# Performance work log

Hardware: AMD Instinct MI355X
Metric: run time of the kernel (lower is better)

Reference implementation:

```python
import jax, jax.numpy as jnp
import numpy as np

H = 2048          # hidden_size
E = 16            # n_routed_experts
K = 4             # num_experts_per_tok
I = 1408          # moe_intermediate_size
SH_I = 2 * I      # shared experts intermediate (n_shared_experts * moe_intermediate_size)
B, S = 1, 1024


def setup_inputs() -> dict:
    key = jax.random.key(0)
    ks = jax.random.split(key, 9)
    sc_h = 1.0 / np.sqrt(H)
    sc_i = 1.0 / np.sqrt(I)
    return {
        "hidden_states": jax.random.normal(ks[0], (B, S, H), dtype=jnp.float32),
        "w_gate": jax.random.normal(ks[1], (E, H), dtype=jnp.float32) * sc_h,
        "wg": jax.random.normal(ks[2], (E, H, I), dtype=jnp.float32) * sc_h,  # gate_proj per expert
        "wu": jax.random.normal(ks[3], (E, H, I), dtype=jnp.float32) * sc_h,  # up_proj per expert
        "wd": jax.random.normal(ks[4], (E, I, H), dtype=jnp.float32) * sc_i,  # down_proj per expert
        "sg": jax.random.normal(ks[5], (H, SH_I), dtype=jnp.float32) * sc_h,  # shared gate_proj
        "su": jax.random.normal(ks[6], (H, SH_I), dtype=jnp.float32) * sc_h,  # shared up_proj
        "sd": jax.random.normal(ks[7], (SH_I, H), dtype=jnp.float32) * (1.0 / np.sqrt(SH_I)),
    }


def reference(hidden_states, w_gate, wg, wu, wd, sg, su, sd):
    b, s, h = hidden_states.shape
    x = hidden_states.reshape(-1, h)                      # [T, H]
    T = x.shape[0]

    # --- router: softmax (fp32) -> topk -> scatter-add weights into [T, E] ---
    logits = x @ w_gate.T                                 # [T, E]
    probs = jax.nn.softmax(logits.astype(jnp.float32), axis=-1)
    top_w, top_i = jax.lax.top_k(probs, K)                # [T, K]
    routing_weight = jnp.zeros((T, E), dtype=probs.dtype)
    routing_weight = routing_weight.at[jnp.arange(T)[:, None], top_i].add(top_w)  # scatter_add_

    # --- routed experts (grouped SwiGLU MLPs), weighted combine ---
    g = jnp.einsum('th,ehi->tei', x, wg)                  # [T, E, I]
    u = jnp.einsum('th,ehi->tei', x, wu)
    act = jax.nn.silu(g) * u                              # [T, E, I]
    routed = jnp.einsum('te,tei,eih->th', routing_weight, act, wd)  # [T, H]

    # --- shared experts (always on) ---
    shared = (jax.nn.silu(x @ sg) * (x @ su)) @ sd        # [T, H]

    out = (routed + shared).astype(hidden_states.dtype)
    return out.reshape(b, s, h)
```

## Files before the change

kernel.cpp:

```cpp
#include <hip/hip_runtime.h>
#include <hip/hip_bf16.h>
#include <stdint.h>

#define T_NUM 1024
#define H_DIM 2048
#define E_NUM 16
#define TOPK 4
#define I_DIM 1408
#define SHI_DIM 2816

typedef __attribute__((ext_vector_type(4))) float f32x4;
typedef __attribute__((ext_vector_type(8))) short bf16x8;
typedef __attribute__((ext_vector_type(4))) short s16x4;

static __device__ __forceinline__ short f2bf(float f) {
    __hip_bfloat16 h = __float2bfloat16(f);
    return __builtin_bit_cast(short, h);
}

__global__ void router_kernel(const float* __restrict__ x, const float* __restrict__ wgate,
                              int* __restrict__ top_e, float* __restrict__ top_w) {
    const int t = blockIdx.x;
    const int tid = threadIdx.x;
    __shared__ float xsh[H_DIM];
    const float* xr = x + (size_t)t * H_DIM;
    for (int h = tid; h < H_DIM; h += 256) xsh[h] = xr[h];
    __syncthreads();

    const int e = tid >> 4;
    const int j = tid & 15;
    const float* wr = wgate + (size_t)e * H_DIM;
    float acc = 0.f;
    for (int h = j; h < H_DIM; h += 16) acc += xsh[h] * wr[h];
    #pragma unroll
    for (int m = 8; m >= 1; m >>= 1) acc += __shfl_down(acc, m, 16);

    __shared__ float logits[E_NUM];
    if (j == 0) logits[e] = acc;
    __syncthreads();

    if (tid == 0) {
        float mx = logits[0];
        #pragma unroll
        for (int i = 1; i < E_NUM; ++i) mx = fmaxf(mx, logits[i]);
        float p[E_NUM]; float s = 0.f;
        #pragma unroll
        for (int i = 0; i < E_NUM; ++i) { p[i] = expf(logits[i] - mx); s += p[i]; }
        const float inv = 1.f / s;
        #pragma unroll
        for (int i = 0; i < E_NUM; ++i) p[i] *= inv;
        for (int k = 0; k < TOPK; ++k) {
            float best = -1.f; int bi = 0;
            #pragma unroll
            for (int i = 0; i < E_NUM; ++i) if (p[i] > best) { best = p[i]; bi = i; }
            top_e[t * TOPK + k] = bi;
            top_w[t * TOPK + k] = best;
            p[bi] = -2.f;
        }
    }
}

__global__ void perm_kernel(const int* __restrict__ top_e,
                            int* __restrict__ offs, int* __restrict__ perm) {
    __shared__ int cnt[256][E_NUM];
    __shared__ int base[E_NUM];
    const int tid = threadIdx.x;
    int c[E_NUM];
    #pragma unroll
    for (int i = 0; i < E_NUM; ++i) c[i] = 0;
    for (int s = tid * 16; s < tid * 16 + 16; ++s) c[top_e[s]]++;
    #pragma unroll
    for (int i = 0; i < E_NUM; ++i) cnt[tid][i] = c[i];
    __syncthreads();
    if (tid < E_NUM) {
        int run = 0;
        for (int b = 0; b < 256; ++b) { int v = cnt[b][tid]; cnt[b][tid] = run; run += v; }
        base[tid] = run;
    }
    __syncthreads();
    if (tid == 0) {
        int run = 0;
        for (int e2 = 0; e2 < E_NUM; ++e2) { int v = base[e2]; base[e2] = run; offs[e2] = run; run += v; }
        offs[E_NUM] = run;
    }
    __syncthreads();
    int run[E_NUM];
    #pragma unroll
    for (int i = 0; i < E_NUM; ++i) run[i] = base[i] + cnt[tid][i];
    for (int s = tid * 16; s < tid * 16 + 16; ++s) {
        int e2 = top_e[s];
        perm[run[e2]++] = s;
    }
}

template<int MODE>
__global__ __launch_bounds__(256, 2) void moe_gemm(
    const float* __restrict__ A, int lda, int Kdim,
    const float* __restrict__ B1g, const float* __restrict__ B2g, int ldb,
    float* __restrict__ Out, int ldo,
    const int* __restrict__ perm, const int* __restrict__ offs,
    const float* __restrict__ top_w)
{
    constexpr int NB = (MODE == 0 || MODE == 1) ? 2 : 1;
    constexpr int BM = 128, BN = 128, BK = 32, KP = 40;
    __shared__ short As[2][BM * KP];
    __shared__ short Bs[2][NB * BN * KP];
    __shared__ int   rows_a[BM];
    __shared__ int   rows_o[BM];
    __shared__ float w_m[BM];

    const int tid = threadIdx.x;
    const int nt = blockIdx.x, mt = blockIdx.y, e = blockIdx.z;

    int off = 0, cnt = T_NUM;
    const float* B1 = B1g;
    const float* B2 = B2g;
    if constexpr (MODE == 0) {
        off = offs[e]; cnt = offs[e + 1] - off;
        if (mt * BM >= cnt) return;
        B1 = B1g + (size_t)e * H_DIM * I_DIM;
        B2 = B2g + (size_t)e * H_DIM * I_DIM;
    }
    if constexpr (MODE == 2) {
        off = offs[e]; cnt = offs[e + 1] - off;
        if (mt * BM >= cnt) return;
        B1 = B1g + (size_t)e * I_DIM * H_DIM;
    }

    if (tid < BM) {
        const int gm = mt * BM + tid;
        if constexpr (MODE == 0) {
            int s = perm[off + (gm < cnt ? gm : cnt - 1)];
            rows_a[tid] = s >> 2; rows_o[tid] = s; w_m[tid] = 1.f;
        } else if constexpr (MODE == 2) {
            int s = perm[off + (gm < cnt ? gm : cnt - 1)];
            rows_a[tid] = s; rows_o[tid] = s >> 2; w_m[tid] = top_w[s];
        } else {
            rows_a[tid] = gm; rows_o[tid] = gm; w_m[tid] = 1.f;
        }
    }
    __syncthreads();

    f32x4 aReg[4];
    float bReg[NB][4][4];

    auto gload = [&](int kt) {
        const int k0 = kt * BK;
        #pragma unroll
        for (int it = 0; it < 4; ++it) {
            const int q = it * 256 + tid;
            const int m = q >> 3, kq = (q & 7) * 4;
            aReg[it] = *reinterpret_cast<const f32x4*>(A + (size_t)rows_a[m] * lda + k0 + kq);
        }
        #pragma unroll
        for (int it = 0; it < 4; ++it) {
            const int q = it * 256 + tid;
            const int n = q & 127, kb = (q >> 7) * 4;
            const float* p1 = B1 + (size_t)(k0 + kb) * ldb + (size_t)nt * BN + n;
            #pragma unroll
            for (int dk = 0; dk < 4; ++dk) bReg[0][it][dk] = p1[(size_t)dk * ldb];
            if constexpr (NB == 2) {
                const float* p2 = B2 + (size_t)(k0 + kb) * ldb + (size_t)nt * BN + n;
                #pragma unroll
                for (int dk = 0; dk < 4; ++dk) bReg[1][it][dk] = p2[(size_t)dk * ldb];
            }
        }
    };

    auto swrite = [&](int buf) {
        #pragma unroll
        for (int it = 0; it < 4; ++it) {
            const int q = it * 256 + tid;
            const int m = q >> 3, kq = (q & 7) * 4;
            s16x4 v = { f2bf(aReg[it][0]), f2bf(aReg[it][1]), f2bf(aReg[it][2]), f2bf(aReg[it][3]) };
            *reinterpret_cast<s16x4*>(&As[buf][m * KP + kq]) = v;
        }
        #pragma unroll
        for (int it = 0; it < 4; ++it) {
            const int q = it * 256 + tid;
            const int n = q & 127, kb = (q >> 7) * 4;
            #pragma unroll
            for (int mat = 0; mat < NB; ++mat) {
                s16x4 v = { f2bf(bReg[mat][it][0]), f2bf(bReg[mat][it][1]),
                            f2bf(bReg[mat][it][2]), f2bf(bReg[mat][it][3]) };
                *reinterpret_cast<s16x4*>(&Bs[buf][mat * BN * KP + n * KP + kb]) = v;
            }
        }
    };

    f32x4 acc1[4][4], acc2[4][4];
    #pragma unroll
    for (int i = 0; i < 4; ++i)
        #pragma unroll
        for (int j = 0; j < 4; ++j) { acc1[i][j] = (f32x4)0.f; acc2[i][j] = (f32x4)0.f; }

    const int lane = tid & 63;
    const int wr = (tid >> 6) >> 1, wc = (tid >> 6) & 1;
    const int lrow = lane & 15;
    const int lko = (lane >> 4) * 8;

    auto compute = [&](int buf) {
        bf16x8 af[4];
        #pragma unroll
        for (int mi = 0; mi < 4; ++mi)
            af[mi] = *reinterpret_cast<const bf16x8*>(&As[buf][(wr * 64 + mi * 16 + lrow) * KP + lko]);
        #pragma unroll
        for (int ni = 0; ni < 4; ++ni) {
            const int brow = (wc * 64 + ni * 16 + lrow) * KP + lko;
            bf16x8 b1 = *reinterpret_cast<const bf16x8*>(&Bs[buf][brow]);
            #pragma unroll
            for (int mi = 0; mi < 4; ++mi)
                acc1[mi][ni] = __builtin_amdgcn_mfma_f32_16x16x32_bf16(af[mi], b1, acc1[mi][ni], 0, 0, 0);
            if constexpr (NB == 2) {
                bf16x8 b2 = *reinterpret_cast<const bf16x8*>(&Bs[buf][BN * KP + brow]);
                #pragma unroll
                for (int mi = 0; mi < 4; ++mi)
                    acc2[mi][ni] = __builtin_amdgcn_mfma_f32_16x16x32_bf16(af[mi], b2, acc2[mi][ni], 0, 0, 0);
            }
        }
    };

    const int NK = Kdim / BK;
    gload(0);
    int cur = 0;
    for (int kt = 0; kt < NK; ++kt) {
        swrite(cur);
        __syncthreads();
        if (kt + 1 < NK) gload(kt + 1);
        compute(cur);
        cur ^= 1;
    }

    #pragma unroll
    for (int mi = 0; mi < 4; ++mi) {
        #pragma unroll
        for (int j = 0; j < 4; ++j) {
            const int ml = wr * 64 + mi * 16 + (lane >> 4) * 4 + j;
            const int gm = mt * BM + ml;
            if constexpr (MODE == 0 || MODE == 2) { if (gm >= cnt) continue; }
            const int orow = rows_o[ml];
            const float wsc = w_m[ml];
            #pragma unroll
            for (int ni = 0; ni < 4; ++ni) {
                const int n = nt * BN + wc * 64 + ni * 16 + (lane & 15);
                const float v1 = acc1[mi][ni][j];
                if constexpr (NB == 2) {
                    const float u = acc2[mi][ni][j];
                    const float s = v1 / (1.f + __expf(-v1));
                    Out[(size_t)orow * ldo + n] = s * u;
                } else if constexpr (MODE == 2) {
                    atomicAdd(&Out[(size_t)orow * ldo + n], v1 * wsc);
                } else {
                    Out[(size_t)orow * ldo + n] = v1;
                }
            }
        }
    }
}

extern "C" void kernel_launch(void* const* d_in, const int* in_sizes, int n_in,
                              void* d_out, int out_size, void* d_ws, size_t ws_size,
                              hipStream_t stream) {
    const float* x     = (const float*)d_in[0];
    const float* wgate = (const float*)d_in[1];
    const float* wg    = (const float*)d_in[2];
    const float* wu    = (const float*)d_in[3];
    const float* wd    = (const float*)d_in[4];
    const float* sg    = (const float*)d_in[5];
    const float* su    = (const float*)d_in[6];
    const float* sd    = (const float*)d_in[7];
    float* out = (float*)d_out;

    uintptr_t p = (uintptr_t)d_ws;
    auto alloc = [&](size_t bytes) {
        p = (p + 255) & ~(uintptr_t)255;
        void* r = (void*)p; p += bytes; return r;
    };
    int*   top_e = (int*)alloc((size_t)T_NUM * TOPK * sizeof(int));
    float* top_w = (float*)alloc((size_t)T_NUM * TOPK * sizeof(float));
    int*   offs  = (int*)alloc((E_NUM + 1) * sizeof(int));
    int*   perm  = (int*)alloc((size_t)T_NUM * TOPK * sizeof(int));
    float* act_r = (float*)alloc((size_t)T_NUM * TOPK * I_DIM * sizeof(float));
    float* act_s = (float*)alloc((size_t)T_NUM * SHI_DIM * sizeof(float));

    router_kernel<<<T_NUM, 256, 0, stream>>>(x, wgate, top_e, top_w);
    perm_kernel<<<1, 256, 0, stream>>>(top_e, offs, perm);

    moe_gemm<1><<<dim3(SHI_DIM / 128, T_NUM / 128, 1), 256, 0, stream>>>(
        x, H_DIM, H_DIM, sg, su, SHI_DIM, act_s, SHI_DIM, nullptr, nullptr, nullptr);
    moe_gemm<3><<<dim3(H_DIM / 128, T_NUM / 128, 1), 256, 0, stream>>>(
        act_s, SHI_DIM, SHI_DIM, sd, nullptr, H_DIM, out, H_DIM, nullptr, nullptr, nullptr);
    moe_gemm<0><<<dim3(I_DIM / 128, T_NUM / 128, E_NUM), 256, 0, stream>>>(
        x, H_DIM, H_DIM, wg, wu, I_DIM, act_r, I_DIM, perm, offs, nullptr);
    moe_gemm<2><<<dim3(H_DIM / 128, T_NUM / 128, E_NUM), 256, 0, stream>>>(
        act_r, I_DIM, I_DIM, wd, nullptr, H_DIM, out, H_DIM, perm, offs, top_w);
}
```

Measured before the change: 582.6 us.

## Pre-convert weights to transposed bf16 and use direct-to-LDS bf16 GEMMs

Adds kernels that transpose and convert all expert and shared weights to bf16 on every call, converts activations to bf16 in the router, and replaces the fused fp32-input GEMMs with bf16 GEMMs. These use global_load_lds with swizzled LDS, XCD-aware block remapping and higher occupancy, plus separate gate/up GEMMs followed by a standalone SwiGLU kernel. The intent is to halve GEMM operand traffic and drop in-loop fp32-to-bf16 conversion. The trade-off is roughly 1.2 GB of extra weight read/write per call for the conversion and extra intermediate buffers. The new path runs only if the workspace is large enough; otherwise the old fp32 path remains, now with an added barrier.

```diff
diff --git a/kernel.cpp b/kernel.cpp
--- a/kernel.cpp
+++ b/kernel.cpp
@@ -17,15 +17,32 @@
     __hip_bfloat16 h = __float2bfloat16(f);
     return __builtin_bit_cast(short, h);
 }
+static __device__ __forceinline__ float bf2f(short s) {
+    return __bfloat162float(__builtin_bit_cast(__hip_bfloat16, s));
+}
+
+static __device__ __forceinline__ void gll16(const short* g, const short* l) {
+    __builtin_amdgcn_global_load_lds(
+        (const __attribute__((address_space(1))) void*)g,
+        (__attribute__((address_space(3))) void*)l, 16, 0, 0);
+}
 
 __global__ void router_kernel(const float* __restrict__ x, const float* __restrict__ wgate,
-                              int* __restrict__ top_e, float* __restrict__ top_w) {
+                              int* __restrict__ top_e, float* __restrict__ top_w,
+                              short* __restrict__ xb) {
     const int t = blockIdx.x;
     const int tid = threadIdx.x;
     __shared__ float xsh[H_DIM];
     const float* xr = x + (size_t)t * H_DIM;
     for (int h = tid; h < H_DIM; h += 256) xsh[h] = xr[h];
     __syncthreads();
+
+    {
+        short v[8];
+        #pragma unroll
+        for (int i = 0; i < 8; ++i) v[i] = f2bf(xsh[tid * 8 + i]);
+        *reinterpret_cast<bf16x8*>(xb + (size_t)t * H_DIM + tid * 8) = *(bf16x8*)v;
+    }
 
     const int e = tid >> 4;
     const int j = tid & 15;
@@ -93,8 +110,189 @@
     }
 }
 
+__global__ void tconv_kernel(const float* __restrict__ src, short* __restrict__ dst,
+                             int R, int C) {
+    __shared__ float t[64][65];
+    const int c0 = blockIdx.x * 64, r0 = blockIdx.y * 64;
+    const size_t mo = (size_t)blockIdx.z * R * C;
+    const float* s = src + mo;
+    short* d = dst + mo;
+    const int tid = threadIdx.x;
+    #pragma unroll
+    for (int it = 0; it < 4; ++it) {
+        const int q = it * 256 + tid;
+        const int r = q >> 4, c4 = (q & 15) * 4;
+        f32x4 v = *reinterpret_cast<const f32x4*>(s + (size_t)(r0 + r) * C + c0 + c4);
+        t[r][c4] = v[0]; t[r][c4 + 1] = v[1]; t[r][c4 + 2] = v[2]; t[r][c4 + 3] = v[3];
+    }
+    __syncthreads();
+    #pragma unroll
+    for (int it = 0; it < 2; ++it) {
+        const int q = it * 256 + tid;
+        const int c = q >> 3, r8 = (q & 7) * 8;
+        short v[8];
+        #pragma unroll
+        for (int i = 0; i < 8; ++i) v[i] = f2bf(t[r8 + i][c]);
+        *reinterpret_cast<bf16x8*>(d + (size_t)(c0 + c) * R + r0 + r8) = *(bf16x8*)v;
+    }
+}
+
+__global__ void swiglu_kernel(const short* __restrict__ g, const short* __restrict__ u,
+                              short* __restrict__ act, int n8) {
+    const int i = blockIdx.x * 256 + threadIdx.x;
+    if (i >= n8) return;
+    bf16x8 gv = *reinterpret_cast<const bf16x8*>(g + (size_t)i * 8);
+    bf16x8 uv = *reinterpret_cast<const bf16x8*>(u + (size_t)i * 8);
+    short o[8];
+    #pragma unroll
+    for (int j = 0; j < 8; ++j) {
+        float gf = bf2f(gv[j]);
+        float uf = bf2f(uv[j]);
+        o[j] = f2bf(gf / (1.f + __expf(-gf)) * uf);
+    }
+    *reinterpret_cast<bf16x8*>(act + (size_t)i * 8) = *(bf16x8*)o;
+}
+
 template<int MODE>
-__global__ __launch_bounds__(256, 2) void moe_gemm(
+__global__ __launch_bounds__(256, 4) void gemm_bf(
+    const short* __restrict__ A, int lda, int Kdim,
+    const short* __restrict__ Bg,
+    void* __restrict__ Outv, int ldo,
+    const int* __restrict__ perm, const int* __restrict__ offs,
+    const float* __restrict__ top_w, int nmt, int nnt)
+{
+    constexpr int BK = 32;
+    __shared__ __align__(16) short As[2][128 * 32];
+    __shared__ __align__(16) short Bs[2][128 * 32];
+    __shared__ int   rows_a[128];
+    __shared__ int   rows_o[128];
+    __shared__ float w_m[128];
+
+    const int tid = threadIdx.x;
+
+    int wg = blockIdx.x;
+    {
+        const int nwg = gridDim.x;
+        const int qq = nwg >> 3, rr = nwg & 7;
+        const int xcd = wg & 7, lin = wg >> 3;
+        wg = (xcd < rr ? xcd * (qq + 1) : rr * (qq + 1) + (xcd - rr) * qq) + lin;
+    }
+    const int mt = wg % nmt;
+    const int nt = (wg / nmt) % nnt;
+    const int e  = wg / (nmt * nnt);
+
+    int off = 0, cnt = T_NUM;
+    const short* Bt = Bg;
+    if constexpr (MODE == 0 || MODE == 2) {
+        off = offs[e]; cnt = offs[e + 1] - off;
+        if (mt * 128 >= cnt) return;
+        Bt = Bg + (size_t)e * ((size_t)nnt * 128) * Kdim;
+    }
+
+    if (tid < 128) {
+        const int gm = mt * 128 + tid;
+        if constexpr (MODE == 0) {
+            int s = perm[off + (gm < cnt ? gm : cnt - 1)];
+            rows_a[tid] = s >> 2; rows_o[tid] = s; w_m[tid] = 1.f;
+        } else if constexpr (MODE == 2) {
+            int s = perm[off + (gm < cnt ? gm : cnt - 1)];
+            rows_a[tid] = s; rows_o[tid] = s >> 2; w_m[tid] = top_w[s];
+        } else {
+            rows_a[tid] = gm; rows_o[tid] = gm; w_m[tid] = 1.f;
+        }
+    }
+    __syncthreads();
+
+    int raReg[2];
+    #pragma unroll
+    for (int it = 0; it < 2; ++it) raReg[it] = rows_a[it * 64 + (tid >> 2)];
+
+    auto stage = [&](int buf, int kt) {
+        const int k0 = kt * BK;
+        #pragma unroll
+        for (int it = 0; it < 2; ++it) {
+            const int q = it * 256 + tid;
+            const int m = q >> 2;
+            const int c = ((q & 3) ^ ((m >> 1) & 3)) * 8;
+            gll16(A + (size_t)raReg[it] * lda + k0 + c, &As[buf][q * 8]);
+        }
+        #pragma unroll
+        for (int it = 0; it < 2; ++it) {
+            const int q = it * 256 + tid;
+            const int n = q >> 2;
+            const int c = ((q & 3) ^ ((n >> 1) & 3)) * 8;
+            gll16(Bt + (size_t)(nt * 128 + n) * Kdim + k0 + c, &Bs[buf][q * 8]);
+        }
+    };
+
+    f32x4 acc[4][4];
+    #pragma unroll
+    for (int i = 0; i < 4; ++i)
+        #pragma unroll
+        for (int j = 0; j < 4; ++j) acc[i][j] = (f32x4)0.f;
+
+    const int lane = tid & 63;
+    const int wr = (tid >> 7), wc = (tid >> 6) & 1;
+    const int lrow = lane & 15;
+    const int cswz = (((lane >> 4) ^ ((lrow >> 1) & 3)) * 8);
+
+    auto compute = [&](int buf) {
+        bf16x8 af[4];
+        #pragma unroll
+        for (int mi = 0; mi < 4; ++mi)
+            af[mi] = *reinterpret_cast<const bf16x8*>(&As[buf][(wr * 64 + mi * 16 + lrow) * 32 + cswz]);
+        #pragma unroll
+        for (int ni = 0; ni < 4; ++ni) {
+            bf16x8 bfr = *reinterpret_cast<const bf16x8*>(&Bs[buf][(wc * 64 + ni * 16 + lrow) * 32 + cswz]);
+            #pragma unroll
+            for (int mi = 0; mi < 4; ++mi)
+                acc[mi][ni] = __builtin_amdgcn_mfma_f32_16x16x32_bf16(af[mi], bfr, acc[mi][ni], 0, 0, 0);
+        }
+    };
+
+    const int NK = Kdim / BK;
+    stage(0, 0);
+    int buf = 0;
+    for (int kt = 0; kt < NK; ++kt) {
+        if (kt + 1 < NK) {
+            stage(buf ^ 1, kt + 1);
+            asm volatile("s_waitcnt vmcnt(4)" ::: "memory");
+        } else {
+            asm volatile("s_waitcnt vmcnt(0)" ::: "memory");
+        }
+        __builtin_amdgcn_s_barrier();
+        compute(buf);
+        __builtin_amdgcn_s_barrier();
+        buf ^= 1;
+    }
+
+    #pragma unroll
+    for (int mi = 0; mi < 4; ++mi) {
+        #pragma unroll
+        for (int j = 0; j < 4; ++j) {
+            const int ml = wr * 64 + mi * 16 + (lane >> 4) * 4 + j;
+            const int gm = mt * 128 + ml;
+            if constexpr (MODE == 0 || MODE == 2) { if (gm >= cnt) continue; }
+            const int orow = (MODE == 0 || MODE == 2) ? rows_o[ml] : gm;
+            const float wsc = w_m[ml];
+            #pragma unroll
+            for (int ni = 0; ni < 4; ++ni) {
+                const int n = nt * 128 + wc * 64 + ni * 16 + (lane & 15);
+                const float v = acc[mi][ni][j];
+                if constexpr (MODE == 0 || MODE == 1) {
+                    ((short*)Outv)[(size_t)orow * ldo + n] = f2bf(v);
+                } else if constexpr (MODE == 2) {
+                    atomicAdd(&((float*)Outv)[(size_t)orow * ldo + n], v * wsc);
+                } else {
+                    ((float*)Outv)[(size_t)orow * ldo + n] = v;
+                }
+            }
+        }
+    }
+}
+
+template<int MODE>
+__global__ __launch_bounds__(256, 2) void moe_gemm_fb(
     const float* __restrict__ A, int lda, int Kdim,
     const float* __restrict__ B1g, const float* __restrict__ B2g, int ldb,
     float* __restrict__ Out, int ldo,
@@ -229,6 +427,7 @@
         if (kt + 1 < NK) gload(kt + 1);
         compute(cur);
         cur ^= 1;
+        __syncthreads();
     }
 
     #pragma unroll
@@ -271,7 +470,8 @@
     const float* sd    = (const float*)d_in[7];
     float* out = (float*)d_out;
 
-    uintptr_t p = (uintptr_t)d_ws;
+    uintptr_t p0 = (uintptr_t)d_ws;
+    uintptr_t p = p0;
     auto alloc = [&](size_t bytes) {
         p = (p + 255) & ~(uintptr_t)255;
         void* r = (void*)p; p += bytes; return r;
@@ -280,18 +480,73 @@
     float* top_w = (float*)alloc((size_t)T_NUM * TOPK * sizeof(float));
     int*   offs  = (int*)alloc((E_NUM + 1) * sizeof(int));
     int*   perm  = (int*)alloc((size_t)T_NUM * TOPK * sizeof(int));
-    float* act_r = (float*)alloc((size_t)T_NUM * TOPK * I_DIM * sizeof(float));
-    float* act_s = (float*)alloc((size_t)T_NUM * SHI_DIM * sizeof(float));
-
-    router_kernel<<<T_NUM, 256, 0, stream>>>(x, wgate, top_e, top_w);
+    short* xb    = (short*)alloc((size_t)T_NUM * H_DIM * 2);
+
+    const size_t wguSz = (size_t)E_NUM * H_DIM * I_DIM * 2;
+    const size_t shSz  = (size_t)H_DIM * SHI_DIM * 2;
+
+    const size_t need = ((size_t)T_NUM * TOPK * 8 + 4096) + (size_t)T_NUM * H_DIM * 2
+                      + 3 * wguSz + 3 * shSz
+                      + 3 * (size_t)T_NUM * TOPK * I_DIM * 2
+                      + 3 * (size_t)T_NUM * SHI_DIM * 2
+                      + (1u << 20);
+
+    router_kernel<<<T_NUM, 256, 0, stream>>>(x, wgate, top_e, top_w, xb);
     perm_kernel<<<1, 256, 0, stream>>>(top_e, offs, perm);
 
-    moe_gemm<1><<<dim3(SHI_DIM / 128, T_NUM / 128, 1), 256, 0, stream>>>(
-        x, H_DIM, H_DIM, sg, su, SHI_DIM, act_s, SHI_DIM, nullptr, nullptr, nullptr);
-    moe_gemm<3><<<dim3(H_DIM / 128, T_NUM / 128, 1), 256, 0, stream>>>(
-        act_s, SHI_DIM, SHI_DIM, sd, nullptr, H_DIM, out, H_DIM, nullptr, nullptr, nullptr);
-    moe_gemm<0><<<dim3(I_DIM / 128, T_NUM / 128, E_NUM), 256, 0, stream>>>(
-        x, H_DIM, H_DIM, wg, wu, I_DIM, act_r, I_DIM, perm, offs, nullptr);
-    moe_gemm<2><<<dim3(H_DIM / 128, T_NUM / 128, E_NUM), 256, 0, stream>>>(
-        act_r, I_DIM, I_DIM, wd, nullptr, H_DIM, out, H_DIM, perm, offs, top_w);
-}
+    if (ws_size >= need) {
+        short* wgT = (short*)alloc(wguSz);
+        short* wuT = (short*)alloc(wguSz);
+        short* wdT = (short*)alloc(wguSz);
+        short* sgT = (short*)alloc(shSz);
+        short* suT = (short*)alloc(shSz);
+        short* sdT = (short*)alloc(shSz);
+        short* g_r = (short*)alloc((size_t)T_NUM * TOPK * I_DIM * 2);
+        short* u_r = (short*)alloc((size_t)T_NUM * TOPK * I_DIM * 2);
+        short* act_r = (short*)alloc((size_t)T_NUM * TOPK * I_DIM * 2);
+        short* g_s = (short*)alloc((size_t)T_NUM * SHI_DIM * 2);
+        short* u_s = (short*)alloc((size_t)T_NUM * SHI_DIM * 2);
+        short* act_s = (short*)alloc((size_t)T_NUM * SHI_DIM * 2);
+
+        tconv_kernel<<<dim3(I_DIM / 64, H_DIM / 64, E_NUM), 256, 0, stream>>>(wg, wgT, H_DIM, I_DIM);
+        tconv_kernel<<<dim3(I_DIM / 64, H_DIM / 64, E_NUM), 256, 0, stream>>>(wu, wuT, H_DIM, I_DIM);
+        tconv_kernel<<<dim3(H_DIM / 64, I_DIM / 64, E_NUM), 256, 0, stream>>>(wd, wdT, I_DIM, H_DIM);
+        tconv_kernel<<<dim3(SHI_DIM / 64, H_DIM / 64, 1), 256, 0, stream>>>(sg, sgT, H_DIM, SHI_DIM);
+        tconv_kernel<<<dim3(SHI_DIM / 64, H_DIM / 64, 1), 256, 0, stream>>>(su, suT, H_DIM, SHI_DIM);
+        tconv_kernel<<<dim3(H_DIM / 64, SHI_DIM / 64, 1), 256, 0, stream>>>(sd, sdT, SHI_DIM, H_DIM);
+
+        const int nmtT = T_NUM / 128;
+        const int nnI = I_DIM / 128;
+        const int nnH = H_DIM / 128;
+        const int nnS = SHI_DIM / 128;
+
+        gemm_bf<1><<<nmtT * nnS, 256, 0, stream>>>(xb, H_DIM, H_DIM, sgT, g_s, SHI_DIM,
+                                                   nullptr, nullptr, nullptr, nmtT, nnS);
+        gemm_bf<1><<<nmtT * nnS, 256, 0, stream>>>(xb, H_DIM, H_DIM, suT, u_s, SHI_DIM,
+                                                   nullptr, nullptr, nullptr, nmtT, nnS);
+        swiglu_kernel<<<(T_NUM * SHI_DIM / 8 + 255) / 256, 256, 0, stream>>>(
+            g_s, u_s, act_s, T_NUM * SHI_DIM / 8);
+        gemm_bf<3><<<nmtT * nnH, 256, 0, stream>>>(act_s, SHI_DIM, SHI_DIM, sdT, out, H_DIM,
+                                                   nullptr, nullptr, nullptr, nmtT, nnH);
+        gemm_bf<0><<<nmtT * nnI * E_NUM, 256, 0, stream>>>(xb, H_DIM, H_DIM, wgT, g_r, I_DIM,
+                                                           perm, offs, nullptr, nmtT, nnI);
+        gemm_bf<0><<<nmtT * nnI * E_NUM, 256, 0, stream>>>(xb, H_DIM, H_DIM, wuT, u_r, I_DIM,
+                                                           perm, offs, nullptr, nmtT, nnI);
+        swiglu_kernel<<<(T_NUM * TOPK * I_DIM / 8 + 255) / 256, 256, 0, stream>>>(
+            g_r, u_r, act_r, T_NUM * TOPK * I_DIM / 8);
+        gemm_bf<2><<<nmtT * nnH * E_NUM, 256, 0, stream>>>(act_r, I_DIM, I_DIM, wdT, out, H_DIM,
+                                                           perm, offs, top_w, nmtT, nnH);
+    } else {
+        float* act_r = (float*)alloc((size_t)T_NUM * TOPK * I_DIM * sizeof(float));
+        float* act_s = (float*)alloc((size_t)T_NUM * SHI_DIM * sizeof(float));
+
+        moe_gemm_fb<1><<<dim3(SHI_DIM / 128, T_NUM / 128, 1), 256, 0, stream>>>(
+            x, H_DIM, H_DIM, sg, su, SHI_DIM, act_s, SHI_DIM, nullptr, nullptr, nullptr);
+        moe_gemm_fb<3><<<dim3(H_DIM / 128, T_NUM / 128, 1), 256, 0, stream>>>(
+            act_s, SHI_DIM, SHI_DIM, sd, nullptr, H_DIM, out, H_DIM, nullptr, nullptr, nullptr);
+        moe_gemm_fb<0><<<dim3(I_DIM / 128, T_NUM / 128, E_NUM), 256, 0, stream>>>(
+            x, H_DIM, H_DIM, wg, wu, I_DIM, act_r, I_DIM, perm, offs, nullptr);
+        moe_gemm_fb<2><<<dim3(H_DIM / 128, T_NUM / 128, E_NUM), 256, 0, stream>>>(
+            act_r, I_DIM, I_DIM, wd, nullptr, H_DIM, out, H_DIM, perm, offs, top_w);
+    }
+}
```

Result: slower. 631.4 us (+8.4%).
